# Kernel tuning notes

Measured on AMD Instinct MI355X. Metric: run time of the kernel, lower is better.

The kernel has to match this reference:

```python
import jax, jax.numpy as jnp
import numpy as np

DIM = 1024
NUM_HEADS = 16
HEAD_DIM = DIM // NUM_HEADS
SCALE = HEAD_DIM ** -0.25
EPS = 1e-5


def layer_norm(x, w, b):
    mu = jnp.mean(x, axis=-1, keepdims=True)
    var = jnp.var(x, axis=-1, keepdims=True)
    return (x - mu) * jax.lax.rsqrt(var + EPS) * w + b


def setup_inputs() -> dict:
    key = jax.random.key(0)
    ks = jax.random.split(key, 10)
    b, l, d = 2, 2048, DIM
    x = jax.random.normal(ks[0], (b, l, d), dtype=jnp.float32)
    # causal mask, broadcastable over heads: [b, 1, l, l]
    causal = jnp.tril(jnp.ones((l, l), dtype=jnp.int32))
    mask = jnp.broadcast_to(causal[None, None], (b, 1, l, l))
    s = 0.02
    return {
        "x": x,
        "mask": mask,
        "ln1_w": jnp.ones((d,), jnp.float32),
        "ln1_b": jnp.zeros((d,), jnp.float32),
        "qkv_w": jax.random.normal(ks[1], (d, 3 * d), jnp.float32) * s,
        "qkv_b": jnp.zeros((3 * d,), jnp.float32),
        "proj_w": jax.random.normal(ks[2], (d, d), jnp.float32) * s,
        "proj_b": jnp.zeros((d,), jnp.float32),
        "ln2_w": jnp.ones((d,), jnp.float32),
        "ln2_b": jnp.zeros((d,), jnp.float32),
        "ffn_w1": jax.random.normal(ks[3], (d, 4 * d), jnp.float32) * s,
        "ffn_b1": jnp.zeros((4 * d,), jnp.float32),
        "ffn_w2": jax.random.normal(ks[4], (4 * d, d), jnp.float32) * s,
        "ffn_b2": jnp.zeros((d,), jnp.float32),
    }


def attention(x, mask, qkv_w, qkv_b, proj_w, proj_b):
    b, l, d = x.shape
    n, c = NUM_HEADS, HEAD_DIM
    qkv = (x @ qkv_w + qkv_b).reshape(b, l, n * 3, c)
    q, k, v = qkv[:, :, :n], qkv[:, :, n:2 * n], qkv[:, :, 2 * n:]
    # scores: [b, n, l, l], scale applied to both q and k (head_dim^-0.25 each)
    attn = jnp.einsum('binc,bjnc->bnij', q * SCALE, k * SCALE)
    attn = jnp.where(mask[:, :, :l, :l] == 0, -jnp.inf, attn)
    attn = jax.nn.softmax(attn.astype(jnp.float32), axis=-1).astype(x.dtype)
    out = jnp.einsum('bnij,bjnc->binc', attn, v).reshape(b, l, d)
    return out @ proj_w + proj_b


def reference(x, mask, ln1_w, ln1_b, qkv_w, qkv_b, proj_w, proj_b,
              ln2_w, ln2_b, ffn_w1, ffn_b1, ffn_w2, ffn_b2):
    h = x + attention(layer_norm(x, ln1_w, ln1_b), mask, qkv_w, qkv_b, proj_w, proj_b)
    y = layer_norm(h, ln2_w, ln2_b)
    ffn = jax.nn.gelu(y @ ffn_w1 + ffn_b1, approximate=False) @ ffn_w2 + ffn_b2
    return h + ffn
```

## Files before the change

kernel.cpp:

```cpp
#include <hip/hip_runtime.h>
#include <hip/hip_bf16.h>
#include <math.h>

typedef __attribute__((ext_vector_type(8))) short bf16x8;
typedef __attribute__((ext_vector_type(4))) float f32x4;
typedef __attribute__((ext_vector_type(4))) unsigned u32x4;

#define MFMA16(a, b, c) __builtin_amdgcn_mfma_f32_16x16x32_bf16((a), (b), (c), 0, 0, 0)

typedef const __attribute__((address_space(1))) void* gas_ptr;
typedef __attribute__((address_space(3))) void* las_ptr;

__device__ __forceinline__ unsigned pack_bf16(float a, float b) {
    unsigned ua = (unsigned)__bfloat16_as_ushort(__float2bfloat16(a));
    unsigned ub = (unsigned)__bfloat16_as_ushort(__float2bfloat16(b));
    return ua | (ub << 16);
}

__global__ __launch_bounds__(256)
void transpose_all(const float* __restrict__ qkv_w, const float* __restrict__ proj_w,
                   const float* __restrict__ ffn_w1, const float* __restrict__ ffn_w2,
                   __hip_bfloat16* __restrict__ wqkv, __hip_bfloat16* __restrict__ wproj,
                   __hip_bfloat16* __restrict__ wff1, __hip_bfloat16* __restrict__ wff2)
{
    const int bid = blockIdx.x;
    const float* in; __hip_bfloat16* out; int K, N, r;
    if (bid < 3072)      { in = qkv_w;  out = wqkv;  K = 1024; N = 3072; r = bid;        }
    else if (bid < 4096) { in = proj_w; out = wproj; K = 1024; N = 1024; r = bid - 3072; }
    else if (bid < 8192) { in = ffn_w1; out = wff1;  K = 1024; N = 4096; r = bid - 4096; }
    else                 { in = ffn_w2; out = wff2;  K = 4096; N = 1024; r = bid - 8192; }
    const int ncols = N >> 5;
    const int n0 = (r % ncols) * 32, k0 = (r / ncols) * 32;

    __shared__ float t[32][33];
    const int tx = threadIdx.x & 31, ty = threadIdx.x >> 5;
    #pragma unroll
    for (int j = 0; j < 32; j += 8)
        t[ty + j][tx] = in[(size_t)(k0 + ty + j) * N + n0 + tx];
    __syncthreads();
    #pragma unroll
    for (int j = 0; j < 32; j += 8)
        out[(size_t)(n0 + ty + j) * K + k0 + tx] = __float2bfloat16(t[tx][ty + j]);
}

__global__ __launch_bounds__(256)
void ln_kernel(const float* __restrict__ in, const float* __restrict__ w,
               const float* __restrict__ b, __hip_bfloat16* __restrict__ out)
{
    const int row = blockIdx.x;
    const int tid = threadIdx.x;
    const float4 v = reinterpret_cast<const float4*>(in + (size_t)row * 1024)[tid];
    float s  = v.x + v.y + v.z + v.w;
    float s2 = v.x * v.x + v.y * v.y + v.z * v.z + v.w * v.w;
    #pragma unroll
    for (int off = 32; off > 0; off >>= 1) {
        s  += __shfl_down(s,  off);
        s2 += __shfl_down(s2, off);
    }
    __shared__ float red[8];
    const int wv = tid >> 6, ln = tid & 63;
    if (ln == 0) { red[wv] = s; red[4 + wv] = s2; }
    __syncthreads();
    s  = red[0] + red[1] + red[2] + red[3];
    s2 = red[4] + red[5] + red[6] + red[7];
    const float mu   = s * (1.0f / 1024.0f);
    const float var  = s2 * (1.0f / 1024.0f) - mu * mu;
    const float rstd = rsqrtf(var + 1e-5f);
    const float4 wv4 = reinterpret_cast<const float4*>(w)[tid];
    const float4 bv4 = reinterpret_cast<const float4*>(b)[tid];
    const size_t o = (size_t)row * 1024 + tid * 4;
    out[o + 0] = __float2bfloat16((v.x - mu) * rstd * wv4.x + bv4.x);
    out[o + 1] = __float2bfloat16((v.y - mu) * rstd * wv4.y + bv4.y);
    out[o + 2] = __float2bfloat16((v.z - mu) * rstd * wv4.z + bv4.z);
    out[o + 3] = __float2bfloat16((v.w - mu) * rstd * wv4.w + bv4.w);
}

template<int MODE>
__global__ __launch_bounds__(256, 3)
void gemm128p(const __hip_bfloat16* __restrict__ A,
              const __hip_bfloat16* __restrict__ Bt,
              const float* __restrict__ bias,
              void* __restrict__ C0, void* __restrict__ C1,
              int N, int K)
{
    constexpr int SLOT = 8192;
    __shared__ __align__(16) __hip_bfloat16 lds[3 * SLOT];

    const int tid  = threadIdx.x;
    const int lane = tid & 63;
    const int w    = tid >> 6;
    const int wr   = w >> 1, wc = w & 1;
    const int fr   = lane & 15, fq = lane >> 4;

    const int nwg = gridDim.x * gridDim.y;
    int flat = blockIdx.y * gridDim.x + blockIdx.x;
    flat = (flat & 7) * (nwg >> 3) + (flat >> 3);
    const int bx = flat % gridDim.x, by = flat / gridDim.x;
    const int m0 = by * 128, n0 = bx * 128;
    const int NT = K >> 5;

    const int prc = w * 8 + (lane >> 3);
    const int ch  = lane & 7;
    const __hip_bfloat16* aS[2];
    const __hip_bfloat16* bS[2];
    #pragma unroll
    for (int j = 0; j < 2; ++j) {
        const int pr  = prc + 32 * j;
        const int v   = ch ^ (pr & 7);
        const int row = 2 * pr + (v >> 2);
        const int col = 8 * (v & 3);
        aS[j] = A  + (size_t)(m0 + row) * K + col;
        bS[j] = Bt + (size_t)(n0 + row) * K + col;
    }

    auto stage = [&](int kt, int s) {
        __hip_bfloat16* LA = &lds[s * SLOT];
        __hip_bfloat16* LB = LA + 4096;
        #pragma unroll
        for (int j = 0; j < 2; ++j) {
            __builtin_amdgcn_global_load_lds((gas_ptr)(const void*)(aS[j] + kt * 32),
                                             (las_ptr)(void*)(LA + w * 512 + j * 2048), 16, 0, 0);
            __builtin_amdgcn_global_load_lds((gas_ptr)(const void*)(bS[j] + kt * 32),
                                             (las_ptr)(void*)(LB + w * 512 + j * 2048), 16, 0, 0);
        }
    };

    f32x4 acc[4][4] = {};

    stage(0, 0);
    stage(1, 1);
    int sl = 0, sp = 2;

    for (int kt = 0; kt < NT; ++kt) {
        if (kt + 1 < NT)
            asm volatile("s_waitcnt vmcnt(4) lgkmcnt(0)" ::: "memory");
        else
            asm volatile("s_waitcnt vmcnt(0) lgkmcnt(0)" ::: "memory");
        __builtin_amdgcn_s_barrier();
        __builtin_amdgcn_sched_barrier(0);

        if (kt + 2 < NT) stage(kt + 2, sp);

        const __hip_bfloat16* LA = &lds[sl * SLOT];
        const __hip_bfloat16* LB = LA + 4096;
        bf16x8 af[4], bg[4];
        #pragma unroll
        for (int m = 0; m < 4; ++m) {
            const int r = wr * 64 + m * 16 + fr;
            af[m] = *reinterpret_cast<const bf16x8*>(
                &LA[(r >> 1) * 64 + (((r & 1) * 32 + fq * 8) ^ (((r >> 1) & 7) * 8))]);
        }
        #pragma unroll
        for (int n = 0; n < 4; ++n) {
            const int r = wc * 64 + n * 16 + fr;
            bg[n] = *reinterpret_cast<const bf16x8*>(
                &LB[(r >> 1) * 64 + (((r & 1) * 32 + fq * 8) ^ (((r >> 1) & 7) * 8))]);
        }

        __builtin_amdgcn_s_setprio(1);
        #pragma unroll
        for (int m = 0; m < 4; ++m)
            #pragma unroll
            for (int n = 0; n < 4; ++n)
                acc[m][n] = MFMA16(af[m], bg[n], acc[m][n]);
        __builtin_amdgcn_s_setprio(0);

        sl = (sl == 2) ? 0 : sl + 1;
        sp = (sp == 2) ? 0 : sp + 1;
    }

    __syncthreads();
    ushort* E = reinterpret_cast<ushort*>(lds);
    auto eaddr = [](int r, int c16) { return r * 128 + (((c16) ^ ((r >> 3) & 15)) << 3); };

    #pragma unroll
    for (int n = 0; n < 4; ++n) {
        const int col = wc * 64 + n * 16 + fr;
        const float bv = bias[n0 + col];
        #pragma unroll
        for (int m = 0; m < 4; ++m) {
            #pragma unroll
            for (int i = 0; i < 4; ++i) {
                const int row = wr * 64 + m * 16 + fq * 4 + i;
                float v = acc[m][n][i] + bv;
                if (MODE == 2) v = 0.5f * v * (1.0f + erff(v * 0.70710678118654752f));
                E[eaddr(row, col >> 3) + (col & 7)] =
                    __bfloat16_as_ushort(__float2bfloat16(v));
            }
        }
    }
    __syncthreads();

    if (MODE == 3 && n0 >= 2048) {
        const int bq    = m0 >> 11;
        const int lbase = m0 & 2047;
        const int hcb   = n0 - 2048;
        #pragma unroll
        for (int p = 0; p < 8; ++p) {
            const int id  = p * 256 + tid;
            const int hcl = id >> 4;
            const int lc  = id & 15;
            u32x4 pkt;
            #pragma unroll
            for (int k2 = 0; k2 < 4; ++k2) {
                const int l0 = lc * 8 + k2 * 2;
                const unsigned a = E[eaddr(l0,     hcl >> 3) + (hcl & 7)];
                const unsigned b = E[eaddr(l0 + 1, hcl >> 3) + (hcl & 7)];
                pkt[k2] = a | (b << 16);
            }
            *reinterpret_cast<u32x4*>(
                &reinterpret_cast<__hip_bfloat16*>(C1)
                    [((size_t)(bq * 1024 + hcb + hcl) << 11) + lbase + lc * 8]) = pkt;
        }
        return;
    }

    const size_t ldC = (MODE == 3) ? 2048 : (size_t)N;
    __hip_bfloat16* Cb = reinterpret_cast<__hip_bfloat16*>(C0);
    #pragma unroll
    for (int p = 0; p < 8; ++p) {
        const int id  = p * 256 + tid;
        const int row = id >> 4;
        const int c16 = id & 15;
        const bf16x8 vv = *reinterpret_cast<const bf16x8*>(&E[eaddr(row, c16)]);
        *reinterpret_cast<bf16x8*>(&Cb[(size_t)(m0 + row) * ldC + n0 + c16 * 8]) = vv;
    }
}

__global__ __launch_bounds__(256, 3)
void gemm_n64(const __hip_bfloat16* __restrict__ A,
              const __hip_bfloat16* __restrict__ Bt,
              const float* __restrict__ bias,
              const float* __restrict__ resid,
              float* __restrict__ C0,
              int N, int K)
{
    constexpr int SLOT = 6144;
    __shared__ __align__(16) __hip_bfloat16 lds[3 * SLOT];

    const int tid  = threadIdx.x;
    const int lane = tid & 63;
    const int w    = tid >> 6;
    const int wr   = w >> 1, wc = w & 1;
    const int fr   = lane & 15, fq = lane >> 4;

    const int nwg = gridDim.x * gridDim.y;
    int flat = blockIdx.y * gridDim.x + blockIdx.x;
    flat = (flat & 7) * (nwg >> 3) + (flat >> 3);
    const int bx = flat % gridDim.x, by = flat / gridDim.x;
    const int m0 = by * 128, n0 = bx * 64;
    const int NT = K >> 5;

    const int prc = w * 8 + (lane >> 3);
    const int ch  = lane & 7;
    const __hip_bfloat16* aS[2];
    #pragma unroll
    for (int j = 0; j < 2; ++j) {
        const int pr  = prc + 32 * j;
        const int v   = ch ^ (pr & 7);
        aS[j] = A + (size_t)(m0 + 2 * pr + (v >> 2)) * K + 8 * (v & 3);
    }
    const __hip_bfloat16* bS;
    {
        const int c  = w * 64 + lane;
        const int pr = c >> 3;
        const int v  = (c & 7) ^ (pr & 7);
        bS = Bt + (size_t)(n0 + 2 * pr + (v >> 2)) * K + 8 * (v & 3);
    }

    auto stage = [&](int kt, int s) {
        __hip_bfloat16* LA = &lds[s * SLOT];
        __hip_bfloat16* LB = LA + 4096;
        #pragma unroll
        for (int j = 0; j < 2; ++j)
            __builtin_amdgcn_global_load_lds((gas_ptr)(const void*)(aS[j] + kt * 32),
                                             (las_ptr)(void*)(LA + w * 512 + j * 2048), 16, 0, 0);
        __builtin_amdgcn_global_load_lds((gas_ptr)(const void*)(bS + kt * 32),
                                         (las_ptr)(void*)(LB + w * 512), 16, 0, 0);
    };

    f32x4 acc[4][2] = {};

    stage(0, 0);
    stage(1, 1);
    int sl = 0, sp = 2;

    for (int kt = 0; kt < NT; ++kt) {
        if (kt + 1 < NT)
            asm volatile("s_waitcnt vmcnt(3) lgkmcnt(0)" ::: "memory");
        else
            asm volatile("s_waitcnt vmcnt(0) lgkmcnt(0)" ::: "memory");
        __builtin_amdgcn_s_barrier();
        __builtin_amdgcn_sched_barrier(0);

        if (kt + 2 < NT) stage(kt + 2, sp);

        const __hip_bfloat16* LA = &lds[sl * SLOT];
        const __hip_bfloat16* LB = LA + 4096;
        bf16x8 af[4], bg[2];
        #pragma unroll
        for (int m = 0; m < 4; ++m) {
            const int r = wr * 64 + m * 16 + fr;
            af[m] = *reinterpret_cast<const bf16x8*>(
                &LA[(r >> 1) * 64 + (((r & 1) * 32 + fq * 8) ^ (((r >> 1) & 7) * 8))]);
        }
        #pragma unroll
        for (int n = 0; n < 2; ++n) {
            const int r = wc * 32 + n * 16 + fr;
            bg[n] = *reinterpret_cast<const bf16x8*>(
                &LB[(r >> 1) * 64 + (((r & 1) * 32 + fq * 8) ^ (((r >> 1) & 7) * 8))]);
        }

        __builtin_amdgcn_s_setprio(1);
        #pragma unroll
        for (int m = 0; m < 4; ++m)
            #pragma unroll
            for (int n = 0; n < 2; ++n)
                acc[m][n] = MFMA16(af[m], bg[n], acc[m][n]);
        __builtin_amdgcn_s_setprio(0);

        sl = (sl == 2) ? 0 : sl + 1;
        sp = (sp == 2) ? 0 : sp + 1;
    }

    #pragma unroll
    for (int n = 0; n < 2; ++n) {
        const int col = n0 + wc * 32 + n * 16 + fr;
        const float bv = bias[col];
        #pragma unroll
        for (int m = 0; m < 4; ++m)
            #pragma unroll
            for (int i = 0; i < 4; ++i) {
                const int row = m0 + wr * 64 + m * 16 + fq * 4 + i;
                C0[(size_t)row * N + col] = acc[m][n][i] + bv + resid[(size_t)row * N + col];
            }
    }
}

__global__ __launch_bounds__(256)
void attn_kernel(const __hip_bfloat16* __restrict__ qk,
                 const __hip_bfloat16* __restrict__ Vt,
                 __hip_bfloat16* __restrict__ out)
{
    const int bid  = blockIdx.x;
    const int xcd  = bid & 7;
    const int rank = bid >> 3;
    const int panel = xcd * 4 + (rank & 3);
    const int qt   = 31 - (rank >> 2);
    const int h = panel & 15, b = panel >> 4;
    const int q0 = qt * 64;

    const int lane = threadIdx.x & 63;
    const int w    = threadIdx.x >> 6;
    const int fr   = lane & 15, fq = lane >> 4;
    const int qrow = q0 + w * 16 + fr;

    __shared__ __align__(16) __hip_bfloat16 Klds[2][64 * 64];
    __shared__ __align__(16) __hip_bfloat16 Vlds[2][64 * 64];

    bf16x8 qf[2];
    {
        const __hip_bfloat16* qp = qk + ((size_t)(b * 2048 + qrow) << 11) + h * 64 + fq * 8;
        qf[0] = *reinterpret_cast<const bf16x8*>(qp);
        qf[1] = *reinterpret_cast<const bf16x8*>(qp + 32);
    }

    const int srow8 = lane >> 3;
    const int sc    = lane & 7;
    const __hip_bfloat16* Kg[2];
    const __hip_bfloat16* Vg[2];
    #pragma unroll
    for (int j = 0; j < 2; ++j) {
        const int r = w * 16 + j * 8 + srow8;
        const int csw = (sc ^ (r & 7)) * 8;
        Kg[j] = qk + ((size_t)(b * 2048 + r) << 11) + 1024 + h * 64 + csw;
        Vg[j] = Vt + ((size_t)(b * 1024 + h * 64 + r) << 11) + csw;
    }

    auto stage = [&](int kv0, int bufi) {
        __hip_bfloat16* KL = &Klds[bufi][0];
        __hip_bfloat16* VL = &Vlds[bufi][0];
        #pragma unroll
        for (int j = 0; j < 2; ++j) {
            __builtin_amdgcn_global_load_lds(
                (gas_ptr)(const void*)(Kg[j] + ((size_t)kv0 << 11)),
                (las_ptr)(void*)&KL[(w * 16 + j * 8) * 64], 16, 0, 0);
            __builtin_amdgcn_global_load_lds(
                (gas_ptr)(const void*)(Vg[j] + kv0),
                (las_ptr)(void*)&VL[(w * 16 + j * 8) * 64], 16, 0, 0);
        }
    };

    const float SC = 0.125f * 1.44269504088896f;
    float m_run = -1e30f, l_run = 0.0f;
    f32x4 o[4] = {};

    const int ntiles = qt + 1;
    stage(0, 0);
    int cur = 0;

    for (int t = 0; t < ntiles; ++t) {
        const int kv0 = t << 6;
        __syncthreads();
        if (t + 1 < ntiles) stage((t + 1) << 6, cur ^ 1);

        const __hip_bfloat16* Kl = &Klds[cur][0];
        const __hip_bfloat16* Vl = &Vlds[cur][0];

        f32x4 s[4] = {};
        #pragma unroll
        for (int n = 0; n < 4; ++n) {
            const int row = n * 16 + fr;
            const int sw = (row & 7) << 3;
            const bf16x8 k0 = *reinterpret_cast<const bf16x8*>(&Kl[row * 64 + ((fq * 8) ^ sw)]);
            const bf16x8 k1 = *reinterpret_cast<const bf16x8*>(&Kl[row * 64 + ((fq * 8 + 32) ^ sw)]);
            s[n] = MFMA16(k0, qf[0], s[n]);
            s[n] = MFMA16(k1, qf[1], s[n]);
        }

        float pm = -1e30f;
        if (t == ntiles - 1) {
            #pragma unroll
            for (int n = 0; n < 4; ++n)
                #pragma unroll
                for (int i = 0; i < 4; ++i) {
                    const int kvp = kv0 + n * 16 + fq * 4 + i;
                    float sv = s[n][i] * SC;
                    sv = (kvp <= qrow) ? sv : -1e30f;
                    s[n][i] = sv;
                    pm = fmaxf(pm, sv);
                }
        } else {
            #pragma unroll
            for (int n = 0; n < 4; ++n)
                #pragma unroll
                for (int i = 0; i < 4; ++i) {
                    const float sv = s[n][i] * SC;
                    s[n][i] = sv;
                    pm = fmaxf(pm, sv);
                }
        }
        pm = fmaxf(pm, __shfl_xor(pm, 16));
        pm = fmaxf(pm, __shfl_xor(pm, 32));
        const float mnew = fmaxf(m_run, pm);
        const float corr = exp2f(m_run - mnew);
        m_run = mnew;

        float rs = 0.0f;
        unsigned pk[8];
        #pragma unroll
        for (int n = 0; n < 4; ++n) {
            const float p0 = exp2f(s[n][0] - mnew);
            const float p1 = exp2f(s[n][1] - mnew);
            const float p2 = exp2f(s[n][2] - mnew);
            const float p3 = exp2f(s[n][3] - mnew);
            rs += (p0 + p1) + (p2 + p3);
            pk[n * 2 + 0] = pack_bf16(p0, p1);
            pk[n * 2 + 1] = pack_bf16(p2, p3);
        }
        rs += __shfl_xor(rs, 16);
        rs += __shfl_xor(rs, 32);
        l_run = l_run * corr + rs;

        #pragma unroll
        for (int i = 0; i < 4; ++i) {
            const float ci = __shfl(corr, fq * 4 + i);
            o[0][i] *= ci; o[1][i] *= ci; o[2][i] *= ci; o[3][i] *= ci;
        }

        u32x4 A0, A1;
        #pragma unroll
        for (int r = 0; r < 4; ++r) {
            const int slx = fr + ((2 * (fq & 1) + (r >> 1)) << 4);
            const unsigned lo0 = __shfl(pk[0 + (r & 1)], slx);
            const unsigned hi0 = __shfl(pk[2 + (r & 1)], slx);
            const unsigned lo1 = __shfl(pk[4 + (r & 1)], slx);
            const unsigned hi1 = __shfl(pk[6 + (r & 1)], slx);
            A0[r] = (fq & 2) ? hi0 : lo0;
            A1[r] = (fq & 2) ? hi1 : lo1;
        }
        const bf16x8 pa0 = __builtin_bit_cast(bf16x8, A0);
        const bf16x8 pa1 = __builtin_bit_cast(bf16x8, A1);

        #pragma unroll
        for (int tt = 0; tt < 4; ++tt) {
            const int row = tt * 16 + fr;
            const int sw = (row & 7) << 3;
            const bf16x8 v0 = *reinterpret_cast<const bf16x8*>(&Vl[row * 64 + ((fq * 8) ^ sw)]);
            const bf16x8 v1 = *reinterpret_cast<const bf16x8*>(&Vl[row * 64 + ((fq * 8 + 32) ^ sw)]);
            o[tt] = MFMA16(pa0, v0, o[tt]);
            o[tt] = MFMA16(pa1, v1, o[tt]);
        }
        cur ^= 1;
    }

    #pragma unroll
    for (int i = 0; i < 4; ++i) {
        const float li  = __shfl(l_run, fq * 4 + i);
        const float inv = 1.0f / li;
        const int row = q0 + w * 16 + fq * 4 + i;
        #pragma unroll
        for (int tt = 0; tt < 4; ++tt)
            out[(size_t)(b * 2048 + row) * 1024 + h * 64 + tt * 16 + fr] =
                __float2bfloat16(o[tt][i] * inv);
    }
}

extern "C" void kernel_launch(void* const* d_in, const int* in_sizes, int n_in,
                              void* d_out, int out_size, void* d_ws, size_t ws_size,
                              hipStream_t stream)
{
    (void)in_sizes; (void)n_in; (void)out_size; (void)ws_size;
    const float* x      = (const float*)d_in[0];
    const float* ln1_w  = (const float*)d_in[2];
    const float* ln1_b  = (const float*)d_in[3];
    const float* qkv_w  = (const float*)d_in[4];
    const float* qkv_b  = (const float*)d_in[5];
    const float* proj_w = (const float*)d_in[6];
    const float* proj_b = (const float*)d_in[7];
    const float* ln2_w  = (const float*)d_in[8];
    const float* ln2_b  = (const float*)d_in[9];
    const float* ffn_w1 = (const float*)d_in[10];
    const float* ffn_b1 = (const float*)d_in[11];
    const float* ffn_w2 = (const float*)d_in[12];
    const float* ffn_b2 = (const float*)d_in[13];
    float* outp = (float*)d_out;

    char* ws = (char*)d_ws;
    size_t off = 0;
    auto take = [&](size_t bytes) -> char* {
        char* p = ws + off;
        off += (bytes + 255) & ~(size_t)255;
        return p;
    };
    __hip_bfloat16* wqkv  = (__hip_bfloat16*)take((size_t)3072 * 1024 * 2);
    __hip_bfloat16* wproj = (__hip_bfloat16*)take((size_t)1024 * 1024 * 2);
    __hip_bfloat16* wff1  = (__hip_bfloat16*)take((size_t)4096 * 1024 * 2);
    __hip_bfloat16* wff2  = (__hip_bfloat16*)take((size_t)1024 * 4096 * 2);
    float*          hbuf  = (float*)take((size_t)4096 * 1024 * 4);
    __hip_bfloat16* xn    = (__hip_bfloat16*)take((size_t)4096 * 1024 * 2);
    __hip_bfloat16* qkb   = (__hip_bfloat16*)take((size_t)4096 * 2048 * 2);
    __hip_bfloat16* Vt    = (__hip_bfloat16*)take((size_t)2048 * 2048 * 2);
    __hip_bfloat16* attn  = (__hip_bfloat16*)take((size_t)4096 * 1024 * 2);
    __hip_bfloat16* ffn1  = qkb;

    transpose_all<<<12288, 256, 0, stream>>>(qkv_w, proj_w, ffn_w1, ffn_w2,
                                             wqkv, wproj, wff1, wff2);
    ln_kernel<<<4096, 256, 0, stream>>>(x, ln1_w, ln1_b, xn);
    gemm128p<3><<<dim3(24, 32), 256, 0, stream>>>(
        xn, wqkv, qkv_b, qkb, Vt, 3072, 1024);
    attn_kernel<<<1024, 256, 0, stream>>>(qkb, Vt, attn);
    gemm_n64<<<dim3(16, 32), 256, 0, stream>>>(
        attn, wproj, proj_b, x, hbuf, 1024, 1024);
    ln_kernel<<<4096, 256, 0, stream>>>(hbuf, ln2_w, ln2_b, xn);
    gemm128p<2><<<dim3(32, 32), 256, 0, stream>>>(
        xn, wff1, ffn_b1, ffn1, nullptr, 4096, 1024);
    gemm_n64<<<dim3(16, 32), 256, 0, stream>>>(
        ffn1, wff2, ffn_b2, hbuf, outp, 1024, 4096);
}
```

Baseline: 244.8 us.

## Add 256x256 FFN1 GEMM, fold QK scale into QKV epilogue, lazy softmax rescale

Replaces the FFN1 GELU GEMM with a new 256x256-tile, 512-thread kernel that uses a 4-deep global_load_lds pipeline and split A-loads, which raises data reuse per tile. The softmax scale (including log2e) is folded into the Q columns in the QKV GEMM epilogue, so the attention kernel no longer multiplies every score. The online softmax now skips the max update and output rescale unless the new max exceeds the running max by more than 8, which removes per-tile corrections. The tradeoff is larger LDS use with one block per CU, plus a possible small loss of precision when the lazy rescale is skipped.

New measurement: 244.2 us. No clear change (-0.2%).

```diff
diff --git a/kernel.cpp b/kernel.cpp
--- a/kernel.cpp
+++ b/kernel.cpp
@@ -10,6 +10,8 @@
 
 typedef const __attribute__((address_space(1))) void* gas_ptr;
 typedef __attribute__((address_space(3))) void* las_ptr;
+
+#define QK_SCALE 0.18033688011112042f
 
 __device__ __forceinline__ unsigned pack_bf16(float a, float b) {
     unsigned ua = (unsigned)__bfloat16_as_ushort(__float2bfloat16(a));
@@ -173,6 +175,7 @@
     ushort* E = reinterpret_cast<ushort*>(lds);
     auto eaddr = [](int r, int c16) { return r * 128 + (((c16) ^ ((r >> 3) & 15)) << 3); };
 
+    const float qsc = (MODE == 3 && n0 < 1024) ? QK_SCALE : 1.0f;
     #pragma unroll
     for (int n = 0; n < 4; ++n) {
         const int col = wc * 64 + n * 16 + fr;
@@ -184,6 +187,7 @@
                 const int row = wr * 64 + m * 16 + fq * 4 + i;
                 float v = acc[m][n][i] + bv;
                 if (MODE == 2) v = 0.5f * v * (1.0f + erff(v * 0.70710678118654752f));
+                if (MODE == 3) v *= qsc;
                 E[eaddr(row, col >> 3) + (col & 7)] =
                     __bfloat16_as_ushort(__float2bfloat16(v));
             }
@@ -224,6 +228,153 @@
         const int c16 = id & 15;
         const bf16x8 vv = *reinterpret_cast<const bf16x8*>(&E[eaddr(row, c16)]);
         *reinterpret_cast<bf16x8*>(&Cb[(size_t)(m0 + row) * ldC + n0 + c16 * 8]) = vv;
+    }
+}
+
+__global__ __launch_bounds__(512, 1)
+void gemm256g(const __hip_bfloat16* __restrict__ A,
+              const __hip_bfloat16* __restrict__ Bt,
+              const float* __restrict__ bias,
+              __hip_bfloat16* __restrict__ C0,
+              int N, int K)
+{
+    constexpr int SLOT = 16384;
+    __shared__ __align__(16) __hip_bfloat16 lds[4 * SLOT];
+
+    const int tid  = threadIdx.x;
+    const int lane = tid & 63;
+    const int w    = tid >> 6;
+    const int wm   = w >> 2, wn = w & 3;
+    const int fr   = lane & 15, fq = lane >> 4;
+
+    const int nwg = gridDim.x * gridDim.y;
+    int flat = blockIdx.y * gridDim.x + blockIdx.x;
+    flat = (flat & 7) * (nwg >> 3) + (flat >> 3);
+    const int bx = flat % gridDim.x, by = flat / gridDim.x;
+    const int m0 = by * 256, n0 = bx * 256;
+    const int NT = K >> 5;
+
+    const __hip_bfloat16* aS[2];
+    const __hip_bfloat16* bS[2];
+    #pragma unroll
+    for (int j = 0; j < 2; ++j) {
+        const int c   = tid + 512 * j;
+        const int row = c >> 2;
+        const int lc  = (c & 3) ^ ((row >> 1) & 3);
+        aS[j] = A  + (size_t)(m0 + row) * K + lc * 8;
+        bS[j] = Bt + (size_t)(n0 + row) * K + lc * 8;
+    }
+
+    auto stageA = [&](int kt) {
+        __hip_bfloat16* L = &lds[(kt & 3) * SLOT];
+        #pragma unroll
+        for (int j = 0; j < 2; ++j)
+            __builtin_amdgcn_global_load_lds((gas_ptr)(const void*)(aS[j] + kt * 32),
+                                             (las_ptr)(void*)(L + w * 512 + j * 4096), 16, 0, 0);
+    };
+    auto stageB = [&](int kt) {
+        __hip_bfloat16* L = &lds[(kt & 3) * SLOT] + 8192;
+        #pragma unroll
+        for (int j = 0; j < 2; ++j)
+            __builtin_amdgcn_global_load_lds((gas_ptr)(const void*)(bS[j] + kt * 32),
+                                             (las_ptr)(void*)(L + w * 512 + j * 4096), 16, 0, 0);
+    };
+
+    f32x4 acc[8][4] = {};
+
+    stageA(0); stageB(0);
+    stageA(1); stageB(1);
+    stageA(2); stageB(2);
+    asm volatile("s_waitcnt vmcnt(8)" ::: "memory");
+    __builtin_amdgcn_s_barrier();
+    __builtin_amdgcn_sched_barrier(0);
+
+    for (int kt = 0; kt < NT; ++kt) {
+        const __hip_bfloat16* LA = &lds[(kt & 3) * SLOT];
+        const __hip_bfloat16* LB = LA + 8192;
+        bf16x8 af[4], bg[4];
+
+        #pragma unroll
+        for (int m = 0; m < 4; ++m) {
+            const int r = wm * 128 + m * 16 + fr;
+            af[m] = *reinterpret_cast<const bf16x8*>(
+                &LA[r * 32 + ((fq ^ ((r >> 1) & 3)) << 3)]);
+        }
+        #pragma unroll
+        for (int n = 0; n < 4; ++n) {
+            const int r = wn * 64 + n * 16 + fr;
+            bg[n] = *reinterpret_cast<const bf16x8*>(
+                &LB[r * 32 + ((fq ^ ((r >> 1) & 3)) << 3)]);
+        }
+        if (kt + 3 < NT) stageA(kt + 3);
+        __builtin_amdgcn_sched_barrier(0);
+        __builtin_amdgcn_s_barrier();
+        asm volatile("s_waitcnt lgkmcnt(0)" ::: "memory");
+        __builtin_amdgcn_sched_barrier(0);
+        __builtin_amdgcn_s_setprio(1);
+        #pragma unroll
+        for (int m = 0; m < 4; ++m)
+            #pragma unroll
+            for (int n = 0; n < 4; ++n)
+                acc[m][n] = MFMA16(af[m], bg[n], acc[m][n]);
+        __builtin_amdgcn_s_setprio(0);
+        __builtin_amdgcn_sched_barrier(0);
+        __builtin_amdgcn_s_barrier();
+
+        #pragma unroll
+        for (int m = 0; m < 4; ++m) {
+            const int r = wm * 128 + 64 + m * 16 + fr;
+            af[m] = *reinterpret_cast<const bf16x8*>(
+                &LA[r * 32 + ((fq ^ ((r >> 1) & 3)) << 3)]);
+        }
+        if (kt + 3 < NT) stageB(kt + 3);
+        __builtin_amdgcn_sched_barrier(0);
+        __builtin_amdgcn_s_barrier();
+        asm volatile("s_waitcnt lgkmcnt(0)" ::: "memory");
+        __builtin_amdgcn_sched_barrier(0);
+        __builtin_amdgcn_s_setprio(1);
+        #pragma unroll
+        for (int m = 0; m < 4; ++m)
+            #pragma unroll
+            for (int n = 0; n < 4; ++n)
+                acc[4 + m][n] = MFMA16(af[m], bg[n], acc[4 + m][n]);
+        __builtin_amdgcn_s_setprio(0);
+        __builtin_amdgcn_sched_barrier(0);
+        if (kt + 3 < NT)      asm volatile("s_waitcnt vmcnt(8)" ::: "memory");
+        else if (kt + 2 < NT) asm volatile("s_waitcnt vmcnt(4)" ::: "memory");
+        else                  asm volatile("s_waitcnt vmcnt(0)" ::: "memory");
+        __builtin_amdgcn_s_barrier();
+    }
+
+    __syncthreads();
+    ushort* E = reinterpret_cast<ushort*>(lds);
+    auto eaddr = [](int r, int c16) { return r * 256 + (((c16) ^ (r & 31)) << 3); };
+
+    #pragma unroll
+    for (int n = 0; n < 4; ++n) {
+        const int col = wn * 64 + n * 16 + fr;
+        const float bv = bias[n0 + col];
+        #pragma unroll
+        for (int a = 0; a < 8; ++a) {
+            #pragma unroll
+            for (int i = 0; i < 4; ++i) {
+                const int row = wm * 128 + (a >> 2) * 64 + (a & 3) * 16 + fq * 4 + i;
+                float v = acc[a][n][i] + bv;
+                v = 0.5f * v * (1.0f + erff(v * 0.70710678118654752f));
+                E[eaddr(row, col >> 3) + (col & 7)] =
+                    __bfloat16_as_ushort(__float2bfloat16(v));
+            }
+        }
+    }
+    __syncthreads();
+
+    #pragma unroll
+    for (int p = 0; p < 16; ++p) {
+        const int id  = p * 512 + tid;
+        const int row = id >> 5;
+        const int c16 = id & 31;
+        const bf16x8 vv = *reinterpret_cast<const bf16x8*>(&E[eaddr(row, c16)]);
+        *reinterpret_cast<bf16x8*>(&C0[(size_t)(m0 + row) * N + n0 + c16 * 8]) = vv;
     }
 }
 
@@ -391,7 +542,6 @@
         }
     };
 
-    const float SC = 0.125f * 1.44269504088896f;
     float m_run = -1e30f, l_run = 0.0f;
     f32x4 o[4] = {};
 
@@ -425,7 +575,7 @@
                 #pragma unroll
                 for (int i = 0; i < 4; ++i) {
                     const int kvp = kv0 + n * 16 + fq * 4 + i;
-                    float sv = s[n][i] * SC;
+                    float sv = s[n][i];
                     sv = (kvp <= qrow) ? sv : -1e30f;
                     s[n][i] = sv;
                     pm = fmaxf(pm, sv);
@@ -434,39 +584,39 @@
             #pragma unroll
             for (int n = 0; n < 4; ++n)
                 #pragma unroll
-                for (int i = 0; i < 4; ++i) {
-                    const float sv = s[n][i] * SC;
-                    s[n][i] = sv;
-                    pm = fmaxf(pm, sv);
-                }
+                for (int i = 0; i < 4; ++i)
+                    pm = fmaxf(pm, s[n][i]);
         }
         pm = fmaxf(pm, __shfl_xor(pm, 16));
         pm = fmaxf(pm, __shfl_xor(pm, 32));
-        const float mnew = fmaxf(m_run, pm);
-        const float corr = exp2f(m_run - mnew);
-        m_run = mnew;
+
+        if (!__all(pm <= m_run + 8.0f)) {
+            const float mnew = fmaxf(m_run, pm);
+            const float corr = exp2f(m_run - mnew);
+            m_run = mnew;
+            l_run *= corr;
+            #pragma unroll
+            for (int i = 0; i < 4; ++i) {
+                const float ci = __shfl(corr, fq * 4 + i);
+                o[0][i] *= ci; o[1][i] *= ci; o[2][i] *= ci; o[3][i] *= ci;
+            }
+        }
 
         float rs = 0.0f;
         unsigned pk[8];
         #pragma unroll
         for (int n = 0; n < 4; ++n) {
-            const float p0 = exp2f(s[n][0] - mnew);
-            const float p1 = exp2f(s[n][1] - mnew);
-            const float p2 = exp2f(s[n][2] - mnew);
-            const float p3 = exp2f(s[n][3] - mnew);
+            const float p0 = exp2f(s[n][0] - m_run);
+            const float p1 = exp2f(s[n][1] - m_run);
+            const float p2 = exp2f(s[n][2] - m_run);
+            const float p3 = exp2f(s[n][3] - m_run);
             rs += (p0 + p1) + (p2 + p3);
             pk[n * 2 + 0] = pack_bf16(p0, p1);
             pk[n * 2 + 1] = pack_bf16(p2, p3);
         }
         rs += __shfl_xor(rs, 16);
         rs += __shfl_xor(rs, 32);
-        l_run = l_run * corr + rs;
-
-        #pragma unroll
-        for (int i = 0; i < 4; ++i) {
-            const float ci = __shfl(corr, fq * 4 + i);
-            o[0][i] *= ci; o[1][i] *= ci; o[2][i] *= ci; o[3][i] *= ci;
-        }
+        l_run += rs;
 
         u32x4 A0, A1;
         #pragma unroll
@@ -553,8 +703,8 @@
     gemm_n64<<<dim3(16, 32), 256, 0, stream>>>(
         attn, wproj, proj_b, x, hbuf, 1024, 1024);
     ln_kernel<<<4096, 256, 0, stream>>>(hbuf, ln2_w, ln2_b, xn);
-    gemm128p<2><<<dim3(32, 32), 256, 0, stream>>>(
-        xn, wff1, ffn_b1, ffn1, nullptr, 4096, 1024);
+    gemm256g<<<dim3(16, 16), 512, 0, stream>>>(
+        xn, wff1, ffn_b1, ffn1, 4096, 1024);
     gemm_n64<<<dim3(16, 32), 256, 0, stream>>>(
         ffn1, wff2, ffn_b2, hbuf, outp, 1024, 4096);
 }
```
